# Performance work log

Measured on AMD Instinct MI355X. Metric: run time of the kernel, lower is better.

The kernel has to match this reference:

```python
import jax, jax.numpy as jnp
import numpy as np
from jax import lax

B, L, D, C = 4096, 50, 128, 64
V = 100000
H = D // 2  # bidirectional LSTM hidden size; 2*H == emb_dim


def setup_inputs() -> dict:
    key = jax.random.key(0)
    ks = jax.random.split(key, 26)
    f = lambda k, s: jax.random.normal(k, s, dtype=jnp.float32) * 0.05
    return {
        "r_idx": jax.random.randint(ks[0], (B,), 0, V),
        "a_idx": jax.random.randint(ks[1], (B,), 0, V),
        "acc_idx": jax.random.randint(ks[2], (B,), 0, V),
        "rank_q": jax.random.normal(ks[3], (B, L, D), dtype=jnp.float32),
        "rank_q_len": jax.random.randint(ks[4], (B,), 0, L),
        "ru_emb": f(ks[5], (V, D)),
        "au_emb": f(ks[6], (V, D)),
        "Wih_f": f(ks[7], (4 * H, D)), "Whh_f": f(ks[8], (4 * H, H)),
        "bih_f": f(ks[9], (4 * H,)), "bhh_f": f(ks[10], (4 * H,)),
        "Wih_b": f(ks[11], (4 * H, D)), "Whh_b": f(ks[12], (4 * H, H)),
        "bih_b": f(ks[13], (4 * H,)), "bhh_b": f(ks[14], (4 * H,)),
        "conv1_w": f(ks[15], (C, 1, D)), "conv1_b": f(ks[16], (C,)),
        "conv2_w": f(ks[17], (C, 2, D)), "conv2_b": f(ks[18], (C,)),
        "conv3_w": f(ks[19], (C, 3, D)), "conv3_b": f(ks[20], (C,)),
        "fc1_w": f(ks[21], (6,)), "fc1_b": f(ks[22], (1,)),
        "fc2_w": f(ks[23], (C,)), "fc2_b": f(ks[24], (1,)),
    }


def _lstm_dir(x, Wih, Whh, bih, bhh, reverse):
    # x: [B, L, D] -> outputs [B, L, H]; PyTorch gate order i,f,g,o
    b = x.shape[0]
    xs = jnp.swapaxes(x, 0, 1)  # [L, B, D]
    h0 = jnp.zeros((b, Whh.shape[1]), x.dtype)

    def step(carry, xt):
        h, c = carry
        gates = xt @ Wih.T + h @ Whh.T + (bih + bhh)
        i, fg, g, o = jnp.split(gates, 4, axis=-1)
        i = jax.nn.sigmoid(i)
        fg = jax.nn.sigmoid(fg)
        g = jnp.tanh(g)
        o = jax.nn.sigmoid(o)
        c = fg * c + i * g
        h = o * jnp.tanh(c)
        return (h, c), h

    _, ys = lax.scan(step, (h0, h0), xs, reverse=reverse)
    return jnp.swapaxes(ys, 0, 1)


def _score(mat, conv1_w, conv1_b, conv2_w, conv2_b, conv3_w, conv3_b, fc1_w, fc1_b, fc2_w, fc2_b):
    # mat: [B, 3, D]; three tiny conv branches (kernel heights 1/2/3, width=D)
    branches = []
    for w, bias in ((conv1_w, conv1_b), (conv2_w, conv2_b), (conv3_w, conv3_b)):
        k = w.shape[1]
        wins = jnp.stack([mat[:, i:i + k] for i in range(3 - k + 1)], axis=1)  # [B, W, k, D]
        branches.append(jax.nn.relu(jnp.einsum('bwkd,ckd->bcw', wins, w) + bias[None, :, None]))
    s = jnp.concatenate(branches, axis=2)  # [B, C, 6]
    h = jnp.einsum('bcw,w->bc', s, fc1_w) + fc1_b[0]  # fc_new_1: 6 -> 1
    return jnp.einsum('bc,c->b', h, fc2_w) + fc2_b[0]  # fc_new_2: C -> 1


def reference(r_idx, a_idx, acc_idx, rank_q, rank_q_len, ru_emb, au_emb,
              Wih_f, Whh_f, bih_f, bhh_f, Wih_b, Whh_b, bih_b, bhh_b,
              conv1_w, conv1_b, conv2_w, conv2_b, conv3_w, conv3_b,
              fc1_w, fc1_b, fc2_w, fc2_b):
    emb_r = ru_emb[r_idx]
    emb_a = au_emb[a_idx]
    emb_acc = au_emb[acc_idx]
    # bidirectional LSTM over the question sequence
    out_f = _lstm_dir(rank_q, Wih_f, Whh_f, bih_f, bhh_f, reverse=False)
    out_b = _lstm_dir(rank_q, Wih_b, Whh_b, bih_b, bhh_b, reverse=True)
    q_out = jnp.concatenate([out_f, out_b], axis=-1)  # [B, L, D]
    # prepend a zero timestep, then gather per-example at index rank_q_len
    q_pad = jnp.concatenate([jnp.zeros((q_out.shape[0], 1, q_out.shape[2]), q_out.dtype), q_out], axis=1)
    emb_q = q_pad[jnp.arange(q_pad.shape[0]), rank_q_len]  # [B, D]
    low = jnp.stack([emb_r, emb_q, emb_a], axis=1)   # [B, 3, D]
    high = jnp.stack([emb_r, emb_q, emb_acc], axis=1)
    fcp = (conv1_w, conv1_b, conv2_w, conv2_b, conv3_w, conv3_b, fc1_w, fc1_b, fc2_w, fc2_b)
    low_s = _score(low, *fcp)
    high_s = _score(high, *fcp)
    return jnp.sum(low_s - high_s)
```

## Files before the change

kernel.cpp:

```cpp
#include <hip/hip_runtime.h>
#include <hip/hip_bf16.h>

#define LSEQ 50
#define BATCH 4096

typedef __attribute__((ext_vector_type(8))) short bf16x8;
typedef __attribute__((ext_vector_type(4))) float f32x4;

__device__ __forceinline__ unsigned short f2bf(float f) {
    unsigned u = __builtin_bit_cast(unsigned, f);
    u += 0x7fffu + ((u >> 16) & 1u);
    return (unsigned short)(u >> 16);
}
__device__ __forceinline__ float fsigm(float x) {
    return __builtin_amdgcn_rcpf(1.0f + __builtin_amdgcn_exp2f(-1.44269504f * x));
}
__device__ __forceinline__ float ftanh(float x) {
    float e = __builtin_amdgcn_exp2f(2.88539008f * x);
    return 1.0f - 2.0f * __builtin_amdgcn_rcpf(e + 1.0f);
}

__global__ __launch_bounds__(256, 2)
void lstm_kernel(const float* __restrict__ rank_q, const int* __restrict__ qlen,
                 const float* __restrict__ Wih_f, const float* __restrict__ Whh_f,
                 const float* __restrict__ bih_f, const float* __restrict__ bhh_f,
                 const float* __restrict__ Wih_b, const float* __restrict__ Whh_b,
                 const float* __restrict__ bih_b, const float* __restrict__ bhh_b,
                 float* __restrict__ embq)
{
    const int blk = blockIdx.x;
    const int dir = blk >> 8;
    const int b0  = (blk & 255) << 4;
    const int tid = threadIdx.x;
    const int wv  = tid >> 6;
    const int ln  = tid & 63;
    const int lm  = ln & 15;
    const int lq  = ln >> 4;
    const int m   = (wv << 4) + lm;

    const float* Wih = dir ? Wih_b : Wih_f;
    const float* Whh = dir ? Whh_b : Whh_f;
    const float* bih = dir ? bih_b : bih_f;
    const float* bhh = dir ? bhh_b : bhh_f;

    __shared__ __align__(16) unsigned short xbuf[2][16][136];
    __shared__ __align__(16) unsigned short hbuf[2][16][72];

    bf16x8 bfrag[4][6];
    float bias[4];
    #pragma unroll
    for (int j = 0; j < 4; ++j) {
        const int n = (j << 6) + m;
        bias[j] = bih[n] + bhh[n];
        #pragma unroll
        for (int s = 0; s < 6; ++s) {
            const int kb = (s << 5) + (lq << 3);
            const float* src = (s < 4) ? (Wih + n * 128 + kb)
                                       : (Whh + n * 64 + (kb - 128));
            float4 w0 = *(const float4*)src;
            float4 w1 = *(const float4*)(src + 4);
            bf16x8 v;
            v[0]=(short)f2bf(w0.x); v[1]=(short)f2bf(w0.y);
            v[2]=(short)f2bf(w0.z); v[3]=(short)f2bf(w0.w);
            v[4]=(short)f2bf(w1.x); v[5]=(short)f2bf(w1.y);
            v[6]=(short)f2bf(w1.z); v[7]=(short)f2bf(w1.w);
            bfrag[j][s] = v;
        }
    }

    int len_e[4];
    #pragma unroll
    for (int r = 0; r < 4; ++r) len_e[r] = qlen[b0 + (lq << 2) + r];

    float cst[4]  = {0.f, 0.f, 0.f, 0.f};
    float qval[4] = {0.f, 0.f, 0.f, 0.f};

    for (int i = tid; i < 16 * 72; i += 256) ((unsigned short*)hbuf)[i] = 0;

    const int se = tid >> 4;
    const int sd = (tid & 15) << 3;
    {
        const int t0 = dir ? (LSEQ - 1) : 0;
        const float* src = rank_q + ((size_t)(b0 + se) * LSEQ + t0) * 128 + sd;
        float4 a = *(const float4*)src;
        float4 b = *(const float4*)(src + 4);
        bf16x8 v;
        v[0]=(short)f2bf(a.x); v[1]=(short)f2bf(a.y); v[2]=(short)f2bf(a.z); v[3]=(short)f2bf(a.w);
        v[4]=(short)f2bf(b.x); v[5]=(short)f2bf(b.y); v[6]=(short)f2bf(b.z); v[7]=(short)f2bf(b.w);
        *(bf16x8*)&xbuf[0][se][sd] = v;
    }
    __syncthreads();

    for (int it = 0; it < LSEQ; ++it) {
        const int t  = dir ? (LSEQ - 1 - it) : it;
        const int rb = it & 1;
        const int wb = rb ^ 1;

        bf16x8 ax0 = *(const bf16x8*)&xbuf[rb][lm][(lq << 3)];
        bf16x8 ax1 = *(const bf16x8*)&xbuf[rb][lm][32 + (lq << 3)];
        bf16x8 ax2 = *(const bf16x8*)&xbuf[rb][lm][64 + (lq << 3)];
        bf16x8 ax3 = *(const bf16x8*)&xbuf[rb][lm][96 + (lq << 3)];
        bf16x8 ah0 = *(const bf16x8*)&hbuf[rb][lm][(lq << 3)];
        bf16x8 ah1 = *(const bf16x8*)&hbuf[rb][lm][32 + (lq << 3)];

        float4 nx0, nx1;
        if (it + 1 < LSEQ) {
            const int tn = dir ? (LSEQ - 2 - it) : (it + 1);
            const float* src = rank_q + ((size_t)(b0 + se) * LSEQ + tn) * 128 + sd;
            nx0 = *(const float4*)src;
            nx1 = *(const float4*)(src + 4);
        }

        f32x4 acc[4];
        #pragma unroll
        for (int j = 0; j < 4; ++j) {
            f32x4 a = {bias[j], bias[j], bias[j], bias[j]};
            a = __builtin_amdgcn_mfma_f32_16x16x32_bf16(ax0, bfrag[j][0], a, 0, 0, 0);
            a = __builtin_amdgcn_mfma_f32_16x16x32_bf16(ax1, bfrag[j][1], a, 0, 0, 0);
            a = __builtin_amdgcn_mfma_f32_16x16x32_bf16(ax2, bfrag[j][2], a, 0, 0, 0);
            a = __builtin_amdgcn_mfma_f32_16x16x32_bf16(ax3, bfrag[j][3], a, 0, 0, 0);
            a = __builtin_amdgcn_mfma_f32_16x16x32_bf16(ah0, bfrag[j][4], a, 0, 0, 0);
            a = __builtin_amdgcn_mfma_f32_16x16x32_bf16(ah1, bfrag[j][5], a, 0, 0, 0);
            acc[j] = a;
        }

        #pragma unroll
        for (int r = 0; r < 4; ++r) {
            float ig = fsigm(acc[0][r]);
            float fg = fsigm(acc[1][r]);
            float gg = ftanh(acc[2][r]);
            float og = fsigm(acc[3][r]);
            float cn = fg * cst[r] + ig * gg;
            cst[r] = cn;
            float hn = og * ftanh(cn);
            if (t == len_e[r] - 1) qval[r] = hn;
            hbuf[wb][(lq << 2) + r][m] = f2bf(hn);
        }

        if (it + 1 < LSEQ) {
            bf16x8 v;
            v[0]=(short)f2bf(nx0.x); v[1]=(short)f2bf(nx0.y); v[2]=(short)f2bf(nx0.z); v[3]=(short)f2bf(nx0.w);
            v[4]=(short)f2bf(nx1.x); v[5]=(short)f2bf(nx1.y); v[6]=(short)f2bf(nx1.z); v[7]=(short)f2bf(nx1.w);
            *(bf16x8*)&xbuf[wb][se][sd] = v;
        }
        __syncthreads();
    }

    #pragma unroll
    for (int r = 0; r < 4; ++r)
        embq[(size_t)(b0 + (lq << 2) + r) * 128 + (dir << 6) + m] = qval[r];
}

__global__ __launch_bounds__(256)
void prep_kernel(const float* __restrict__ c1w, const float* __restrict__ c2w,
                 const float* __restrict__ c3w, float* __restrict__ T)
{
    const int id = blockIdx.x * 256 + threadIdx.x;
    const int m  = id >> 13;
    const int rem = id & 8191;
    const int j  = rem >> 8;
    const int q  = rem & 255;
    const int c  = q >> 2;
    const int d  = (j << 2) + (q & 3);
    const float* src;
    switch (m) {
        case 0:  src = c1w + c * 128 + d;       break;
        case 1:  src = c2w + c * 256 + d;       break;
        case 2:  src = c2w + c * 256 + 128 + d; break;
        case 3:  src = c3w + c * 384 + d;       break;
        case 4:  src = c3w + c * 384 + 128 + d; break;
        default: src = c3w + c * 384 + 256 + d; break;
    }
    T[id] = *src;
}

__global__ __launch_bounds__(256)
void score_kernel(const int* __restrict__ r_idx, const int* __restrict__ a_idx,
                  const int* __restrict__ acc_idx,
                  const float* __restrict__ ru, const float* __restrict__ au,
                  const float* __restrict__ embq, const float* __restrict__ T,
                  const float* __restrict__ c1b, const float* __restrict__ c2b,
                  const float* __restrict__ c3b,
                  const float* __restrict__ fc1w, const float* __restrict__ fc2w,
                  float* __restrict__ diff)
{
    const int tid = threadIdx.x;
    const int wv  = tid >> 6;
    const int c   = tid & 63;
    const int b0  = blockIdx.x << 4;

    __shared__ __align__(16) float emb[64][132];
    {
        const int row = tid & 63;
        const int e   = row >> 2, v = row & 3;
        const int seg = (tid >> 6) << 5;
        const int bb  = b0 + e;
        const float* src = (v == 0) ? ru   + (size_t)r_idx[bb]   * 128 :
                           (v == 1) ? embq + (size_t)bb          * 128 :
                           (v == 2) ? au   + (size_t)a_idx[bb]   * 128 :
                                      au   + (size_t)acc_idx[bb] * 128;
        #pragma unroll
        for (int i = 0; i < 8; ++i) {
            float4 x = *(const float4*)(src + seg + (i << 2));
            *(float4*)&emb[row][seg + (i << 2)] = x;
        }
    }
    __syncthreads();

    float acc[4][9];
    #pragma unroll
    for (int e = 0; e < 4; ++e)
        #pragma unroll
        for (int k = 0; k < 9; ++k) acc[e][k] = 0.f;

    const float4* Tq = (const float4*)T;
    for (int j = 0; j < 32; ++j) {
        const float4* wq = Tq + j * 64 + c;
        const float4 w1  = wq[0];
        const float4 w20 = wq[2048];
        const float4 w21 = wq[4096];
        const float4 w30 = wq[6144];
        const float4 w31 = wq[8192];
        const float4 w32 = wq[10240];
        const int jd = j << 2;
        #pragma unroll
        for (int e = 0; e < 4; ++e) {
            const int br = ((wv << 2) + e) << 2;
            const float4 er = *(const float4*)&emb[br + 0][jd];
            const float4 eq = *(const float4*)&emb[br + 1][jd];
            const float4 ea = *(const float4*)&emb[br + 2][jd];
            const float4 ex = *(const float4*)&emb[br + 3][jd];
            acc[e][0] += w1.x*ea.x  + w1.y*ea.y  + w1.z*ea.z  + w1.w*ea.w;
            acc[e][1] += w1.x*ex.x  + w1.y*ex.y  + w1.z*ex.z  + w1.w*ex.w;
            acc[e][2] += w20.x*eq.x + w20.y*eq.y + w20.z*eq.z + w20.w*eq.w;
            acc[e][3] += w21.x*ea.x + w21.y*ea.y + w21.z*ea.z + w21.w*ea.w;
            acc[e][4] += w21.x*ex.x + w21.y*ex.y + w21.z*ex.z + w21.w*ex.w;
            acc[e][5] += w30.x*er.x + w30.y*er.y + w30.z*er.z + w30.w*er.w;
            acc[e][6] += w31.x*eq.x + w31.y*eq.y + w31.z*eq.z + w31.w*eq.w;
            acc[e][7] += w32.x*ea.x + w32.y*ea.y + w32.z*ea.z + w32.w*ea.w;
            acc[e][8] += w32.x*ex.x + w32.y*ex.y + w32.z*ex.z + w32.w*ex.w;
        }
    }

    const float b1 = c1b[c], b2 = c2b[c], b3 = c3b[c], f2 = fc2w[c];
    const float f12 = fc1w[2], f14 = fc1w[4], f15 = fc1w[5];
    #pragma unroll
    for (int e = 0; e < 4; ++e) {
        const float r1 = fmaxf(acc[e][0] + b1, 0.f) - fmaxf(acc[e][1] + b1, 0.f);
        const float r2 = fmaxf(acc[e][2] + acc[e][3] + b2, 0.f)
                       - fmaxf(acc[e][2] + acc[e][4] + b2, 0.f);
        const float r3 = fmaxf(acc[e][5] + acc[e][6] + acc[e][7] + b3, 0.f)
                       - fmaxf(acc[e][5] + acc[e][6] + acc[e][8] + b3, 0.f);
        float term = f2 * (f12 * r1 + f14 * r2 + f15 * r3);
        #pragma unroll
        for (int off = 32; off; off >>= 1) term += __shfl_down(term, off);
        if (c == 0) diff[b0 + (wv << 2) + e] = term;
    }
}

__global__ void reduce_kernel(const float* __restrict__ diff, float* __restrict__ out)
{
    __shared__ float s[256];
    const int tid = threadIdx.x;
    float v = 0.f;
    for (int i = tid; i < BATCH; i += 256) v += diff[i];
    s[tid] = v;
    __syncthreads();
    for (int st = 128; st > 0; st >>= 1) {
        if (tid < st) s[tid] += s[tid + st];
        __syncthreads();
    }
    if (tid == 0) out[0] = s[0];
}

extern "C" void kernel_launch(void* const* d_in, const int* in_sizes, int n_in,
                              void* d_out, int out_size, void* d_ws, size_t ws_size,
                              hipStream_t stream) {
    (void)in_sizes; (void)n_in; (void)out_size; (void)ws_size;
    const int*   r_idx   = (const int*)d_in[0];
    const int*   a_idx   = (const int*)d_in[1];
    const int*   acc_idx = (const int*)d_in[2];
    const float* rank_q  = (const float*)d_in[3];
    const int*   qlen    = (const int*)d_in[4];
    const float* ru      = (const float*)d_in[5];
    const float* au      = (const float*)d_in[6];
    const float* Wih_f   = (const float*)d_in[7];
    const float* Whh_f   = (const float*)d_in[8];
    const float* bih_f   = (const float*)d_in[9];
    const float* bhh_f   = (const float*)d_in[10];
    const float* Wih_b   = (const float*)d_in[11];
    const float* Whh_b   = (const float*)d_in[12];
    const float* bih_b   = (const float*)d_in[13];
    const float* bhh_b   = (const float*)d_in[14];
    const float* c1w     = (const float*)d_in[15];
    const float* c1b     = (const float*)d_in[16];
    const float* c2w     = (const float*)d_in[17];
    const float* c2b     = (const float*)d_in[18];
    const float* c3w     = (const float*)d_in[19];
    const float* c3b     = (const float*)d_in[20];
    const float* fc1w    = (const float*)d_in[21];
    const float* fc2w    = (const float*)d_in[23];

    float* embq = (float*)d_ws;
    float* diff = embq + (size_t)BATCH * 128;
    float* T    = diff + BATCH;

    prep_kernel<<<192, 256, 0, stream>>>(c1w, c2w, c3w, T);
    lstm_kernel<<<512, 256, 0, stream>>>(rank_q, qlen, Wih_f, Whh_f, bih_f, bhh_f,
                                         Wih_b, Whh_b, bih_b, bhh_b, embq);
    score_kernel<<<BATCH / 16, 256, 0, stream>>>(r_idx, a_idx, acc_idx, ru, au, embq, T,
                                                 c1b, c2b, c3b, fc1w, fc2w, diff);
    reduce_kernel<<<1, 256, 0, stream>>>(diff, (float*)d_out);
}
```

Baseline: 108.4 us.

## Software-pipeline LSTM input projection one step ahead and use hardware bf16 pack

Splits the per-step gate computation so the input-projection MFMAs (x·Wih + bias) for step t+1 run while the recurrent h·Whh MFMAs and gate activations for step t are processed. The x staging buffer becomes triple-buffered with a two-step-ahead global prefetch. The software round-to-nearest-even bf16 conversion is replaced with the v_cvt_pk_bf16_f32 instruction. The goal is to shorten the serial critical path per timestep, at the cost of more registers and LDS, which may lower occupancy.

```diff
diff --git a/kernel.cpp b/kernel.cpp
--- a/kernel.cpp
+++ b/kernel.cpp
@@ -7,10 +7,16 @@
 typedef __attribute__((ext_vector_type(8))) short bf16x8;
 typedef __attribute__((ext_vector_type(4))) float f32x4;
 
-__device__ __forceinline__ unsigned short f2bf(float f) {
-    unsigned u = __builtin_bit_cast(unsigned, f);
-    u += 0x7fffu + ((u >> 16) & 1u);
-    return (unsigned short)(u >> 16);
+__device__ __forceinline__ unsigned cvtpk(float lo, float hi) {
+    unsigned r;
+    asm("v_cvt_pk_bf16_f32 %0, %1, %2" : "=v"(r) : "v"(lo), "v"(hi));
+    return r;
+}
+__device__ __forceinline__ bf16x8 pack8(float4 a, float4 b) {
+    uint4 u;
+    u.x = cvtpk(a.x, a.y); u.y = cvtpk(a.z, a.w);
+    u.z = cvtpk(b.x, b.y); u.w = cvtpk(b.z, b.w);
+    return __builtin_bit_cast(bf16x8, u);
 }
 __device__ __forceinline__ float fsigm(float x) {
     return __builtin_amdgcn_rcpf(1.0f + __builtin_amdgcn_exp2f(-1.44269504f * x));
@@ -43,7 +49,7 @@
     const float* bih = dir ? bih_b : bih_f;
     const float* bhh = dir ? bhh_b : bhh_f;
 
-    __shared__ __align__(16) unsigned short xbuf[2][16][136];
+    __shared__ __align__(16) unsigned short xbuf[3][16][136];
     __shared__ __align__(16) unsigned short hbuf[2][16][72];
 
     bf16x8 bfrag[4][6];
@@ -57,14 +63,7 @@
             const int kb = (s << 5) + (lq << 3);
             const float* src = (s < 4) ? (Wih + n * 128 + kb)
                                        : (Whh + n * 64 + (kb - 128));
-            float4 w0 = *(const float4*)src;
-            float4 w1 = *(const float4*)(src + 4);
-            bf16x8 v;
-            v[0]=(short)f2bf(w0.x); v[1]=(short)f2bf(w0.y);
-            v[2]=(short)f2bf(w0.z); v[3]=(short)f2bf(w0.w);
-            v[4]=(short)f2bf(w1.x); v[5]=(short)f2bf(w1.y);
-            v[6]=(short)f2bf(w1.z); v[7]=(short)f2bf(w1.w);
-            bfrag[j][s] = v;
+            bfrag[j][s] = pack8(*(const float4*)src, *(const float4*)(src + 4));
         }
     }
 
@@ -79,71 +78,99 @@
 
     const int se = tid >> 4;
     const int sd = (tid & 15) << 3;
+    const int tstep = dir ? -128 : 128;
+    const float* gp = rank_q + ((size_t)(b0 + se) * LSEQ + (dir ? LSEQ - 1 : 0)) * 128 + sd;
+
     {
-        const int t0 = dir ? (LSEQ - 1) : 0;
-        const float* src = rank_q + ((size_t)(b0 + se) * LSEQ + t0) * 128 + sd;
-        float4 a = *(const float4*)src;
-        float4 b = *(const float4*)(src + 4);
-        bf16x8 v;
-        v[0]=(short)f2bf(a.x); v[1]=(short)f2bf(a.y); v[2]=(short)f2bf(a.z); v[3]=(short)f2bf(a.w);
-        v[4]=(short)f2bf(b.x); v[5]=(short)f2bf(b.y); v[6]=(short)f2bf(b.z); v[7]=(short)f2bf(b.w);
-        *(bf16x8*)&xbuf[0][se][sd] = v;
+        float4 a0 = *(const float4*)gp, b0v = *(const float4*)(gp + 4); gp += tstep;
+        float4 a1 = *(const float4*)gp, b1v = *(const float4*)(gp + 4); gp += tstep;
+        *(bf16x8*)&xbuf[0][se][sd] = pack8(a0, b0v);
+        *(bf16x8*)&xbuf[1][se][sd] = pack8(a1, b1v);
     }
     __syncthreads();
 
-    for (int it = 0; it < LSEQ; ++it) {
-        const int t  = dir ? (LSEQ - 1 - it) : it;
-        const int rb = it & 1;
-        const int wb = rb ^ 1;
-
-        bf16x8 ax0 = *(const bf16x8*)&xbuf[rb][lm][(lq << 3)];
-        bf16x8 ax1 = *(const bf16x8*)&xbuf[rb][lm][32 + (lq << 3)];
-        bf16x8 ax2 = *(const bf16x8*)&xbuf[rb][lm][64 + (lq << 3)];
-        bf16x8 ax3 = *(const bf16x8*)&xbuf[rb][lm][96 + (lq << 3)];
-        bf16x8 ah0 = *(const bf16x8*)&hbuf[rb][lm][(lq << 3)];
-        bf16x8 ah1 = *(const bf16x8*)&hbuf[rb][lm][32 + (lq << 3)];
-
-        float4 nx0, nx1;
-        if (it + 1 < LSEQ) {
-            const int tn = dir ? (LSEQ - 2 - it) : (it + 1);
-            const float* src = rank_q + ((size_t)(b0 + se) * LSEQ + tn) * 128 + sd;
-            nx0 = *(const float4*)src;
-            nx1 = *(const float4*)(src + 4);
-        }
-
-        f32x4 acc[4];
+    const int xoff = lm * 136 + (lq << 3);
+    const int hoff = lm * 72 + (lq << 3);
+
+    f32x4 accx[4];
+    {
+        const unsigned short* xb = &xbuf[0][0][0];
+        bf16x8 x0 = *(const bf16x8*)(xb + xoff);
+        bf16x8 x1 = *(const bf16x8*)(xb + xoff + 32);
+        bf16x8 x2 = *(const bf16x8*)(xb + xoff + 64);
+        bf16x8 x3 = *(const bf16x8*)(xb + xoff + 96);
         #pragma unroll
         for (int j = 0; j < 4; ++j) {
             f32x4 a = {bias[j], bias[j], bias[j], bias[j]};
-            a = __builtin_amdgcn_mfma_f32_16x16x32_bf16(ax0, bfrag[j][0], a, 0, 0, 0);
-            a = __builtin_amdgcn_mfma_f32_16x16x32_bf16(ax1, bfrag[j][1], a, 0, 0, 0);
-            a = __builtin_amdgcn_mfma_f32_16x16x32_bf16(ax2, bfrag[j][2], a, 0, 0, 0);
-            a = __builtin_amdgcn_mfma_f32_16x16x32_bf16(ax3, bfrag[j][3], a, 0, 0, 0);
-            a = __builtin_amdgcn_mfma_f32_16x16x32_bf16(ah0, bfrag[j][4], a, 0, 0, 0);
-            a = __builtin_amdgcn_mfma_f32_16x16x32_bf16(ah1, bfrag[j][5], a, 0, 0, 0);
-            acc[j] = a;
-        }
-
+            a = __builtin_amdgcn_mfma_f32_16x16x32_bf16(x0, bfrag[j][0], a, 0, 0, 0);
+            a = __builtin_amdgcn_mfma_f32_16x16x32_bf16(x1, bfrag[j][1], a, 0, 0, 0);
+            a = __builtin_amdgcn_mfma_f32_16x16x32_bf16(x2, bfrag[j][2], a, 0, 0, 0);
+            a = __builtin_amdgcn_mfma_f32_16x16x32_bf16(x3, bfrag[j][3], a, 0, 0, 0);
+            accx[j] = a;
+        }
+    }
+
+    int r1 = 1, w2 = 2;
+    for (int it = 0; it < LSEQ; ++it) {
+        const int t   = dir ? (LSEQ - 1 - it) : it;
+        const int rbh = it & 1;
+        const int wbh = rbh ^ 1;
+
+        float4 nxa, nxb;
+        const bool pf = (it <= LSEQ - 3);
+        if (pf) { nxa = *(const float4*)gp; nxb = *(const float4*)(gp + 4); gp += tstep; }
+
+        const unsigned short* hb = &hbuf[rbh][0][0];
+        bf16x8 ah0 = *(const bf16x8*)(hb + hoff);
+        bf16x8 ah1 = *(const bf16x8*)(hb + hoff + 32);
+        f32x4 gate[4];
+        #pragma unroll
+        for (int j = 0; j < 4; ++j) {
+            f32x4 a = __builtin_amdgcn_mfma_f32_16x16x32_bf16(ah0, bfrag[j][4], accx[j], 0, 0, 0);
+            gate[j]  = __builtin_amdgcn_mfma_f32_16x16x32_bf16(ah1, bfrag[j][5], a, 0, 0, 0);
+        }
+
+        if (it + 1 < LSEQ) {
+            const unsigned short* xb = &xbuf[r1][0][0];
+            bf16x8 x0 = *(const bf16x8*)(xb + xoff);
+            bf16x8 x1 = *(const bf16x8*)(xb + xoff + 32);
+            bf16x8 x2 = *(const bf16x8*)(xb + xoff + 64);
+            bf16x8 x3 = *(const bf16x8*)(xb + xoff + 96);
+            #pragma unroll
+            for (int j = 0; j < 4; ++j) {
+                f32x4 a = {bias[j], bias[j], bias[j], bias[j]};
+                a = __builtin_amdgcn_mfma_f32_16x16x32_bf16(x0, bfrag[j][0], a, 0, 0, 0);
+                a = __builtin_amdgcn_mfma_f32_16x16x32_bf16(x1, bfrag[j][1], a, 0, 0, 0);
+                a = __builtin_amdgcn_mfma_f32_16x16x32_bf16(x2, bfrag[j][2], a, 0, 0, 0);
+                a = __builtin_amdgcn_mfma_f32_16x16x32_bf16(x3, bfrag[j][3], a, 0, 0, 0);
+                accx[j] = a;
+            }
+        }
+
+        float hn[4];
         #pragma unroll
         for (int r = 0; r < 4; ++r) {
-            float ig = fsigm(acc[0][r]);
-            float fg = fsigm(acc[1][r]);
-            float gg = ftanh(acc[2][r]);
-            float og = fsigm(acc[3][r]);
+            float ig = fsigm(gate[0][r]);
+            float fg = fsigm(gate[1][r]);
+            float gg = ftanh(gate[2][r]);
+            float og = fsigm(gate[3][r]);
             float cn = fg * cst[r] + ig * gg;
             cst[r] = cn;
-            float hn = og * ftanh(cn);
-            if (t == len_e[r] - 1) qval[r] = hn;
-            hbuf[wb][(lq << 2) + r][m] = f2bf(hn);
-        }
-
-        if (it + 1 < LSEQ) {
-            bf16x8 v;
-            v[0]=(short)f2bf(nx0.x); v[1]=(short)f2bf(nx0.y); v[2]=(short)f2bf(nx0.z); v[3]=(short)f2bf(nx0.w);
-            v[4]=(short)f2bf(nx1.x); v[5]=(short)f2bf(nx1.y); v[6]=(short)f2bf(nx1.z); v[7]=(short)f2bf(nx1.w);
-            *(bf16x8*)&xbuf[wb][se][sd] = v;
-        }
+            hn[r] = og * ftanh(cn);
+            if (t == len_e[r] - 1) qval[r] = hn[r];
+        }
+        const unsigned u01 = cvtpk(hn[0], hn[1]);
+        const unsigned u23 = cvtpk(hn[2], hn[3]);
+        hbuf[wbh][(lq << 2) + 0][m] = (unsigned short)u01;
+        hbuf[wbh][(lq << 2) + 1][m] = (unsigned short)(u01 >> 16);
+        hbuf[wbh][(lq << 2) + 2][m] = (unsigned short)u23;
+        hbuf[wbh][(lq << 2) + 3][m] = (unsigned short)(u23 >> 16);
+
+        if (pf) *(bf16x8*)&xbuf[w2][se][sd] = pack8(nxa, nxb);
+
         __syncthreads();
+        r1 = (r1 == 2) ? 0 : r1 + 1;
+        w2 = (w2 == 2) ? 0 : w2 + 1;
     }
 
     #pragma unroll
```

New measurement: 96.77 us. -10.7%, faster.
